# Kernel optimization log

Measured on AMD Instinct MI355X. Metric: run time of the kernel, lower is better.

## Reference

```python
import jax, jax.numpy as jnp
import numpy as np

EPS = 1e-5
KH = KW = 3
PAD = 1

def conv3x3(x, w, b=None):
    out = jax.lax.conv_general_dilated(
        x, w, window_strides=(1, 1), padding=((PAD, PAD), (PAD, PAD)),
        dimension_numbers=("NCHW", "OIHW", "NCHW"))
    if b is not None:
        out = out + b[None, :, None, None]
    return out

def batchnorm(x, gamma, beta):
    # training-mode BatchNorm2d: batch statistics over (N, H, W)
    mean = x.mean(axis=(0, 2, 3), keepdims=True)
    var = x.var(axis=(0, 2, 3), keepdims=True)
    return gamma[None, :, None, None] * (x - mean) / jnp.sqrt(var + EPS) + beta[None, :, None, None]

def bilinear_gather(x, y_pos, x_pos):
    # x: [B,C,H,W]; y_pos/x_pos: [B,P,H,W] (P = KH*KW sampling taps)
    # zero padding outside image (mmcv modulated deform conv semantics)
    B, C, H, W = x.shape
    P = y_pos.shape[1]
    x_flat = x.reshape(B, C, H * W)
    y0 = jnp.floor(y_pos)
    x0 = jnp.floor(x_pos)
    ly = y_pos - y0
    lx = x_pos - x0
    out = jnp.zeros((B, C, P, H, W), dtype=x.dtype)
    for dy, dx, wgt in ((0, 0, (1 - ly) * (1 - lx)), (0, 1, (1 - ly) * lx),
                        (1, 0, ly * (1 - lx)), (1, 1, ly * lx)):
        yi = y0 + dy
        xi = x0 + dx
        valid = ((yi >= 0) & (yi <= H - 1) & (xi >= 0) & (xi <= W - 1)).astype(x.dtype)
        yc = jnp.clip(yi, 0, H - 1).astype(jnp.int32)
        xc = jnp.clip(xi, 0, W - 1).astype(jnp.int32)
        idx = (yc * W + xc).reshape(B, 1, P * H * W)
        vals = jnp.take_along_axis(x_flat, jnp.broadcast_to(idx, (B, C, P * H * W)), axis=2)
        vals = vals.reshape(B, C, P, H, W)
        out = out + vals * (wgt * valid)[:, None]
    return out  # [B,C,P,H,W]

def modulated_deform_conv(x, w_off, b_off, w_dcn):
    B, C, H, W = x.shape
    P = KH * KW
    off = conv3x3(x, w_off, b_off)  # [B, 3*P, H, W]
    o1, o2, m = jnp.split(off, 3, axis=1)
    offset = jnp.concatenate([o1, o2], axis=1)            # [B, 2P, H, W]
    offset = offset.reshape(B, P, 2, H, W)                # channel 2p -> dy, 2p+1 -> dx
    mask = jax.nn.sigmoid(m)                              # [B, P, H, W]
    hh = jnp.arange(H, dtype=x.dtype)
    ww = jnp.arange(W, dtype=x.dtype)
    ky = jnp.arange(KH, dtype=x.dtype)
    kx = jnp.arange(KW, dtype=x.dtype)
    # base sampling grid per tap p = ky*KW + kx: (h - PAD + ky, w - PAD + kx)
    base_y = (hh[None, :] - PAD + ky[:, None])            # [KH, H]
    base_x = (ww[None, :] - PAD + kx[:, None])            # [KW, W]
    base_y = jnp.broadcast_to(base_y[:, None, :, None], (KH, KW, H, W)).reshape(P, H, W)
    base_x = jnp.broadcast_to(base_x[None, :, None, :], (KH, KW, H, W)).reshape(P, H, W)
    y_pos = base_y[None] + offset[:, :, 0]                # [B,P,H,W]
    x_pos = base_x[None] + offset[:, :, 1]
    sampled = bilinear_gather(x, y_pos, x_pos)            # [B,C,P,H,W]
    sampled = sampled * mask[:, None]
    w = w_dcn.reshape(w_dcn.shape[0], C, P)               # [O, C, P]
    return jnp.einsum("bcphw,ocp->bohw", sampled, w)

def setup_inputs() -> dict:
    key = jax.random.key(0)
    ks = jax.random.split(key, 10)
    B, Ch, H, W = 4, 256, 64, 64
    Cin, Cout = 2 * Ch, 256
    P = KH * KW
    inp = {
        "input_v": jax.random.normal(ks[0], (B, Ch, H, W), jnp.float32),
        "input_i": jax.random.normal(ks[1], (B, Ch, H, W), jnp.float32),
        "w_off": jax.random.normal(ks[2], (3 * P, Cin, KH, KW), jnp.float32) * 0.01,
        "b_off": jnp.zeros((3 * P,), jnp.float32),
        "w_dcn": jax.random.normal(ks[3], (Cout, Cin, KH, KW), jnp.float32) * (1.0 / np.sqrt(Cin * P)),
        "gamma1": jnp.ones((Cout,), jnp.float32),
        "beta1": jnp.zeros((Cout,), jnp.float32),
        "w2": jax.random.normal(ks[4], (Cout, Cout, KH, KW), jnp.float32) * (1.0 / np.sqrt(Cout * P)),
        "gamma2": jnp.ones((Cout,), jnp.float32),
        "beta2": jnp.zeros((Cout,), jnp.float32),
    }
    return inp

def reference(input_v, input_i, w_off, b_off, w_dcn, gamma1, beta1, w2, gamma2, beta2):
    x = jnp.concatenate([input_v, input_i], axis=1)
    out = modulated_deform_conv(x, w_off, b_off, w_dcn)
    out = jax.nn.relu(batchnorm(out, gamma1, beta1))
    out = jax.nn.relu(batchnorm(conv3x3(out, w2), gamma2, beta2))
    return out
```

## Files before the change

### kernel.cpp

```cpp
#include <hip/hip_runtime.h>
#include <cstdint>
#include <cstddef>

typedef unsigned short u16;
typedef __attribute__((ext_vector_type(8))) short s16x8;
typedef __attribute__((ext_vector_type(4))) float f32x4;

#define DEV __device__ __forceinline__

DEV float bf2f(short u){
  union { unsigned int i; float f; } v;
  v.i = ((unsigned int)(u16)u) << 16;
  return v.f;
}
DEV short f2bf(float f){
  union { float f; unsigned int i; } v; v.f = f;
  unsigned int u = v.i;
  u += 0x7fffu + ((u >> 16) & 1u);
  return (short)(u >> 16);
}
DEV s16x8 s16x8_zero(){
  s16x8 z;
#pragma unroll
  for(int j=0;j<8;j++) z[j]=0;
  return z;
}
DEV f32x4 f32x4_zero(){
  f32x4 z;
#pragma unroll
  for(int j=0;j<4;j++) z[j]=0.f;
  return z;
}
DEV f32x4 mfma16(s16x8 a, s16x8 b, f32x4 c){
  return __builtin_amdgcn_mfma_f32_16x16x32_bf16(a, b, c, 0, 0, 0);
}
DEV void bar_lds(){
  asm volatile("s_waitcnt lgkmcnt(0)");
  __builtin_amdgcn_s_barrier();
}
DEV void wait_vm4(){ asm volatile("s_waitcnt vmcnt(4)" ::: "memory"); }
DEV void wait_vm1(){ asm volatile("s_waitcnt vmcnt(1)" ::: "memory"); }
DEV void gload16(const u16* g, u16* l){
  __builtin_amdgcn_global_load_lds(
      (const __attribute__((address_space(1))) unsigned int*)g,
      (__attribute__((address_space(3))) unsigned int*)l, 16, 0, 0);
}

static constexpr size_t OFF_ACC_B  = 0;
static constexpr size_t STATS_B    = 2097152;
static constexpr size_t ZERO_BYTES = STATS_B + 4096;
static constexpr size_t OUT1_ACC_B = ZERO_BYTES;
static constexpr size_t OUT2_ACC_B = OUT1_ACC_B + 16777216;
static constexpr size_t XN_B       = OUT2_ACC_B + 16777216;
static constexpr size_t OUT1N_B    = XN_B + 16777216;
static constexpr size_t WOFFT_B    = OUT1N_B + 8388608;
static constexpr size_t WDCNT_B    = WOFFT_B + 294912;
static constexpr size_t W2T_B      = WDCNT_B + 2359296;

__global__ void k_x_to_nhwc(const float* __restrict__ v, const float* __restrict__ vi,
                            u16* __restrict__ xn){
  __shared__ float tile[64][65];
  const int b = blockIdx.z, c0 = blockIdx.y*64, hw0 = blockIdx.x*64;
  const float* src = (c0 < 256) ? (v  + ((size_t)b*256 + c0)      *4096)
                                : (vi + ((size_t)b*256 + (c0-256))*4096);
  const int t = threadIdx.x;
#pragma unroll
  for(int k=0;k<16;k++){
    int idx = t + k*256;
    int cl = idx >> 6, wl = idx & 63;
    tile[cl][wl] = src[(size_t)cl*4096 + hw0 + wl];
  }
  __syncthreads();
#pragma unroll
  for(int k=0;k<16;k++){
    int idx = t + k*256;
    int wl = idx >> 6, cl = idx & 63;
    xn[(size_t)(b*4096 + hw0 + wl)*512 + c0 + cl] = (u16)f2bf(tile[cl][wl]);
  }
}

__global__ void k_prep_woff(const float* __restrict__ w, u16* __restrict__ wt){
  int idx = blockIdx.x*256 + threadIdx.x;
  if(idx >= 32*4608) return;
  int n = idx / 4608, k = idx % 4608;
  int t = k >> 9, c = k & 511;
  float val = (n < 27) ? w[(size_t)(n*512 + c)*9 + t] : 0.f;
  wt[idx] = (u16)f2bf(val);
}
__global__ void k_prep_wdcn(const float* __restrict__ w, u16* __restrict__ wt){
  int idx = blockIdx.x*256 + threadIdx.x;
  if(idx >= 256*4608) return;
  int n = idx / 4608, k = idx % 4608;
  int t = k >> 9, c = k & 511;
  wt[idx] = (u16)f2bf(w[(size_t)(n*512 + c)*9 + t]);
}
__global__ void k_prep_w2(const float* __restrict__ w, u16* __restrict__ wt){
  int idx = blockIdx.x*256 + threadIdx.x;
  if(idx >= 256*2304) return;
  int n = idx / 2304, k = idx % 2304;
  int t = k >> 8, c = k & 255;
  wt[idx] = (u16)f2bf(w[(size_t)(n*256 + c)*9 + t]);
}

__global__ __launch_bounds__(256, 2) void k_conv_off(
    const u16* __restrict__ xn, const u16* __restrict__ wt, float* __restrict__ offa){
  __shared__ short A_lds[4][128][8];
  __shared__ short B_lds[4][32][8];
  const int tid = threadIdx.x;
  const int lane = tid & 63, wid = tid >> 6;
  const int quad = lane >> 4, ln = lane & 15;
  const int m0 = blockIdx.x * 128;
  const int b = m0 >> 12;
  const int h0 = (m0 & 4095) >> 6;
  const int ks = blockIdx.y;
  const int ts0 = (ks == 3) ? 6 : ks*2;
  const int ntap = (ks == 3) ? 3 : 2;
  const int m_base = wid * 32;
  const int r = tid >> 1, sp = (tid & 1) * 2;
  const int h_r = h0 + (r >> 6), w_r = r & 63;
  const s16x8* Ap = (const s16x8*)A_lds;
  const s16x8* Bp = (const s16x8*)B_lds;
  f32x4 acc[2][2];
#pragma unroll
  for(int mf=0;mf<2;mf++)
#pragma unroll
    for(int nf=0;nf<2;nf++) acc[mf][nf] = f32x4_zero();

  auto load_it = [&](int it, s16x8& v0, s16x8& v1, s16x8& bv){
    const int tp = ts0 + (it >> 4);
    const int cA = (it & 15)*32;
    const int ty = tp/3, tx = tp - ty*3;
    const int y = h_r - 1 + ty, x = w_r - 1 + tx;
    const bool vld = (y>=0) & (y<64) & (x>=0) & (x<64);
    v0 = s16x8_zero(); v1 = s16x8_zero();
    if(vld){
      const u16* src = xn + ((size_t)((b<<12) + (y<<6) + x) << 9) + cA + sp*8;
      v0 = *(const s16x8*)(src);
      v1 = *(const s16x8*)(src + 8);
    }
    if(tid < 128){
      const int n = tid & 31, s2 = tid >> 5;
      bv = *(const s16x8*)(wt + (size_t)n*4608 + tp*512 + cA + s2*8);
    }
  };

  const int NIT = ntap * 16;
  s16x8 v0a, v1a, bva, v0b, v1b, bvb;
  bva = s16x8_zero(); bvb = s16x8_zero();
  load_it(0, v0a, v1a, bva);
  load_it(1, v0b, v1b, bvb);
  for(int it = 0; it < NIT; it += 2){
    bar_lds();
    *(s16x8*)(&A_lds[sp][r][0])   = v0a;
    *(s16x8*)(&A_lds[sp+1][r][0]) = v1a;
    if(tid < 128){
      const int n = tid & 31, s2 = tid >> 5;
      *(s16x8*)(&B_lds[s2][n][0]) = bva;
    }
    if(it + 2 < NIT) load_it(it + 2, v0a, v1a, bva);
    bar_lds();
    {
      s16x8 a0 = Ap[quad*128 + m_base + ln];
      s16x8 a1 = Ap[quad*128 + m_base + 16 + ln];
      s16x8 b0 = Bp[quad*32 + ln];
      s16x8 b1 = Bp[quad*32 + 16 + ln];
      acc[0][0] = mfma16(a0, b0, acc[0][0]);
      acc[0][1] = mfma16(a0, b1, acc[0][1]);
      acc[1][0] = mfma16(a1, b0, acc[1][0]);
      acc[1][1] = mfma16(a1, b1, acc[1][1]);
    }
    bar_lds();
    *(s16x8*)(&A_lds[sp][r][0])   = v0b;
    *(s16x8*)(&A_lds[sp+1][r][0]) = v1b;
    if(tid < 128){
      const int n = tid & 31, s2 = tid >> 5;
      *(s16x8*)(&B_lds[s2][n][0]) = bvb;
    }
    if(it + 3 < NIT) load_it(it + 3, v0b, v1b, bvb);
    bar_lds();
    {
      s16x8 a0 = Ap[quad*128 + m_base + ln];
      s16x8 a1 = Ap[quad*128 + m_base + 16 + ln];
      s16x8 b0 = Bp[quad*32 + ln];
      s16x8 b1 = Bp[quad*32 + 16 + ln];
      acc[0][0] = mfma16(a0, b0, acc[0][0]);
      acc[0][1] = mfma16(a0, b1, acc[0][1]);
      acc[1][0] = mfma16(a1, b0, acc[1][0]);
      acc[1][1] = mfma16(a1, b1, acc[1][1]);
    }
  }
#pragma unroll
  for(int mf=0;mf<2;mf++)
#pragma unroll
    for(int nf=0;nf<2;nf++){
      const int col = nf*16 + ln;
#pragma unroll
      for(int i=0;i<4;i++){
        const int row = m_base + mf*16 + quad*4 + i;
        unsafeAtomicAdd(offa + (size_t)(m0+row)*32 + col, acc[mf][nf][i]);
      }
    }
}

__global__ __launch_bounds__(512, 1) void k_dcn(
    const u16* __restrict__ xn, const u16* __restrict__ wt,
    const float* __restrict__ offa, const float* __restrict__ boff,
    float* __restrict__ outa){
  __shared__ short A_lds[2][8][64][8];
  __shared__ short B_lds[2][8][256][8];
  __shared__ int   p_ofs[9][4][64];
  __shared__ float p_wgt[9][4][64];
  const int tid = threadIdx.x;
  const int lane = tid & 63, wid = tid >> 6;
  const int quad = lane >> 4, ln = lane & 15;
  const int wm = wid >> 2, wn = wid & 3;
  const int m0 = blockIdx.x * 64;
  const int b = m0 >> 12;
  const int h = (m0 & 4095) >> 6;
  const int r_s = tid >> 3, sub = tid & 7;
  constexpr int NP = 72;
  f32x4 acc[2][4];
#pragma unroll
  for(int mf=0;mf<2;mf++)
#pragma unroll
    for(int nf=0;nf<4;nf++) acc[mf][nf] = f32x4_zero();

  {
    const int rr = tid & 63;
    const float* orow = offa + (size_t)(m0+rr)*32;
    for(int tp = tid >> 6; tp < 9; tp += 8){
      float dy = orow[2*tp]   + boff[2*tp];
      float dx = orow[2*tp+1] + boff[2*tp+1];
      float mz = orow[18+tp]  + boff[18+tp];
      float mk = 1.f / (1.f + expf(-mz));
      float ypos = (float)(h - 1 + tp/3) + dy;
      float xpos = (float)(rr - 1 + tp%3) + dx;
      float y0f = floorf(ypos), x0f = floorf(xpos);
      float ly = ypos - y0f, lx = xpos - x0f;
      int y0 = (int)y0f, x0 = (int)x0f;
#pragma unroll
      for(int k=0;k<4;k++){
        int ddy = k >> 1, ddx = k & 1;
        int yi = y0 + ddy, xi = x0 + ddx;
        bool vv = (yi >= 0) & (yi < 64) & (xi >= 0) & (xi < 64);
        float wk = (ddy ? ly : 1.f-ly) * (ddx ? lx : 1.f-lx) * mk;
        if(!vv) wk = 0.f;
        int yc = yi < 0 ? 0 : (yi > 63 ? 63 : yi);
        int xc = xi < 0 ? 0 : (xi > 63 ? 63 : xi);
        p_ofs[tp][k][rr] = ((b << 12) + (yc << 6) + xc) << 9;
        p_wgt[tp][k][rr] = wk;
      }
    }
  }
  __syncthreads();

  auto gather = [&](int t, s16x8* g){
    const int tp = t >> 3;
    const int kcc = (t & 7)*64 + sub*8;
#pragma unroll
    for(int k=0;k<4;k++)
      g[k] = *(const s16x8*)(xn + p_ofs[tp][k][r_s] + kcc);
  };
  auto blendw = [&](int t, const s16x8* g){
    const int tp = t >> 3;
    const float w0 = p_wgt[tp][0][r_s], w1 = p_wgt[tp][1][r_s];
    const float w2 = p_wgt[tp][2][r_s], w3 = p_wgt[tp][3][r_s];
    s16x8 pk;
#pragma unroll
    for(int j=0;j<8;j++){
      float f = w0 * bf2f(g[0][j]);
      f = fmaf(w1, bf2f(g[1][j]), f);
      f = fmaf(w2, bf2f(g[2][j]), f);
      f = fmaf(w3, bf2f(g[3][j]), f);
      pk[j] = f2bf(f);
    }
    return pk;
  };
  auto stageB = [&](int t, int bi){
    const int tp = t >> 3, kc = (t & 7)*64;
#pragma unroll
    for(int i=0;i<4;i++){
      const int li = wid*4 + i;
      const int sl = li >> 2, n0 = (li & 3)*64;
      gload16(wt + (size_t)(n0 + lane)*4608 + tp*512 + kc + sl*8,
              (u16*)&B_lds[bi][sl][n0][0]);
    }
  };
  auto phase = [&](int t, int cur, const s16x8* gB, s16x8* gF){
    const int nxt = cur ^ 1;
    if(t + 1 < NP){
      s16x8 pk = blendw(t + 1, gB);
      *(s16x8*)&A_lds[nxt][sub][r_s][0] = pk;
      stageB(t + 1, nxt);
    }
    __builtin_amdgcn_sched_barrier(0);
    if(t + 2 < NP) gather(t + 2, gF);
#pragma unroll
    for(int kk=0;kk<2;kk++){
      s16x8 af0 = *(const s16x8*)&A_lds[cur][kk*4+quad][wm*32 + ln][0];
      s16x8 af1 = *(const s16x8*)&A_lds[cur][kk*4+quad][wm*32 + 16 + ln][0];
      s16x8 bf[4];
#pragma unroll
      for(int nf=0;nf<4;nf++)
        bf[nf] = *(const s16x8*)&B_lds[cur][kk*4+quad][wn*64 + nf*16 + ln][0];
#pragma unroll
      for(int nf=0;nf<4;nf++){
        acc[0][nf] = mfma16(af0, bf[nf], acc[0][nf]);
        acc[1][nf] = mfma16(af1, bf[nf], acc[1][nf]);
      }
    }
    wait_vm4();
    bar_lds();
  };

  s16x8 S0[4], S1[4];
  gather(0, S0);
  stageB(0, 0);
  __builtin_amdgcn_sched_barrier(0);
  gather(1, S1);
  {
    s16x8 pk = blendw(0, S0);
    *(s16x8*)&A_lds[0][sub][r_s][0] = pk;
  }
  wait_vm4();
  bar_lds();

  for(int t = 0; t < NP; t += 2){
    phase(t,     0, S1, S0);
    phase(t + 1, 1, S0, S1);
  }

#pragma unroll
  for(int mf=0;mf<2;mf++)
#pragma unroll
    for(int nf=0;nf<4;nf++){
      const int col = wn*64 + nf*16 + ln;
#pragma unroll
      for(int i=0;i<4;i++){
        const int row = m0 + wm*32 + mf*16 + quad*4 + i;
        outa[(size_t)row*256 + col] = acc[mf][nf][i];
      }
    }
}

__global__ __launch_bounds__(512, 1) void k_conv2(
    const u16* __restrict__ a_in, const u16* __restrict__ wt, float* __restrict__ outa){
  __shared__ short A_lds[2][8][64][8];
  __shared__ short B_lds[2][8][256][8];
  const int tid = threadIdx.x;
  const int lane = tid & 63, wid = tid >> 6;
  const int quad = lane >> 4, ln = lane & 15;
  const int wm = wid >> 2, wn = wid & 3;
  const int m0 = blockIdx.x * 64;
  const int b = m0 >> 12;
  const int h = (m0 & 4095) >> 6;
  const int r_s = tid >> 3, sub = tid & 7;
  constexpr int NP = 36;
  f32x4 acc[2][4];
#pragma unroll
  for(int mf=0;mf<2;mf++)
#pragma unroll
    for(int nf=0;nf<4;nf++) acc[mf][nf] = f32x4_zero();

  auto loadA = [&](int t, s16x8& va){
    const int tp = t >> 2;
    const int ty = tp/3, tx = tp - ty*3;
    const int y = h - 1 + ty, x = r_s - 1 + tx;
    const bool vld = (y>=0) & (y<64) & (x>=0) & (x<64);
    va = s16x8_zero();
    if(vld)
      va = *(const s16x8*)(a_in + (((size_t)((b<<12) + (y<<6) + x)) << 8)
                           + (t & 3)*64 + sub*8);
  };
  auto stageB = [&](int t, int bi){
    const int tp = t >> 2, kc = (t & 3)*64;
#pragma unroll
    for(int i=0;i<4;i++){
      const int li = wid*4 + i;
      const int sl = li >> 2, n0 = (li & 3)*64;
      gload16(wt + (size_t)(n0 + lane)*2304 + tp*256 + kc + sl*8,
              (u16*)&B_lds[bi][sl][n0][0]);
    }
  };
  auto phase = [&](int t, int cur, const s16x8& vB, s16x8& vF){
    const int nxt = cur ^ 1;
    if(t + 1 < NP){
      *(s16x8*)&A_lds[nxt][sub][r_s][0] = vB;
      stageB(t + 1, nxt);
    }
    __builtin_amdgcn_sched_barrier(0);
    if(t + 2 < NP) loadA(t + 2, vF);
#pragma unroll
    for(int kk=0;kk<2;kk++){
      s16x8 af0 = *(const s16x8*)&A_lds[cur][kk*4+quad][wm*32 + ln][0];
      s16x8 af1 = *(const s16x8*)&A_lds[cur][kk*4+quad][wm*32 + 16 + ln][0];
      s16x8 bf[4];
#pragma unroll
      for(int nf=0;nf<4;nf++)
        bf[nf] = *(const s16x8*)&B_lds[cur][kk*4+quad][wn*64 + nf*16 + ln][0];
#pragma unroll
      for(int nf=0;nf<4;nf++){
        acc[0][nf] = mfma16(af0, bf[nf], acc[0][nf]);
        acc[1][nf] = mfma16(af1, bf[nf], acc[1][nf]);
      }
    }
    wait_vm1();
    bar_lds();
  };

  s16x8 S0, S1;
  loadA(0, S0);
  stageB(0, 0);
  __builtin_amdgcn_sched_barrier(0);
  loadA(1, S1);
  *(s16x8*)&A_lds[0][sub][r_s][0] = S0;
  wait_vm1();
  bar_lds();

  for(int t = 0; t < NP; t += 2){
    phase(t,     0, S1, S0);
    phase(t + 1, 1, S0, S1);
  }

#pragma unroll
  for(int mf=0;mf<2;mf++)
#pragma unroll
    for(int nf=0;nf<4;nf++){
      const int col = wn*64 + nf*16 + ln;
#pragma unroll
      for(int i=0;i<4;i++){
        const int row = m0 + wm*32 + mf*16 + quad*4 + i;
        outa[(size_t)row*256 + col] = acc[mf][nf][i];
      }
    }
}

__global__ void k_stats(const float* __restrict__ acc, float* __restrict__ sum,
                        float* __restrict__ sq){
  const int m0 = blockIdx.x*64;
  const int c = threadIdx.x;
  float s = 0.f, q = 0.f;
  for(int i=0;i<64;i++){
    float v = acc[(size_t)(m0+i)*256 + c];
    s += v; q += v*v;
  }
  unsafeAtomicAdd(sum + c, s);
  unsafeAtomicAdd(sq + c, q);
}

__global__ void k_bn1(const float* __restrict__ acc, const float* __restrict__ sum,
                      const float* __restrict__ sq, const float* __restrict__ g,
                      const float* __restrict__ bt, u16* __restrict__ o){
  __shared__ float sc[256], sh[256];
  const int t = threadIdx.x;
  {
    float mean = sum[t] * (1.f/16384.f);
    float var  = sq[t] * (1.f/16384.f) - mean*mean;
    float rstd = rsqrtf(var + 1e-5f);
    float s = g[t] * rstd;
    sc[t] = s; sh[t] = bt[t] - mean*s;
  }
  __syncthreads();
  const int c4 = (t & 63) * 4;
  const float s0 = sc[c4], s1 = sc[c4+1], s2 = sc[c4+2], s3 = sc[c4+3];
  const float h0 = sh[c4], h1 = sh[c4+1], h2 = sh[c4+2], h3 = sh[c4+3];
#pragma unroll
  for(int k=0;k<4;k++){
    int m = blockIdx.x*16 + k*4 + (t>>6);
    const float4 v = *(const float4*)(acc + (size_t)m*256 + c4);
    unsigned int lo = (unsigned int)(u16)f2bf(fmaxf(0.f, v.x*s0 + h0))
                    | ((unsigned int)(u16)f2bf(fmaxf(0.f, v.y*s1 + h1)) << 16);
    unsigned int hi = (unsigned int)(u16)f2bf(fmaxf(0.f, v.z*s2 + h2))
                    | ((unsigned int)(u16)f2bf(fmaxf(0.f, v.w*s3 + h3)) << 16);
    uint2 pr; pr.x = lo; pr.y = hi;
    *(uint2*)(o + (size_t)m*256 + c4) = pr;
  }
}

__global__ void k_bn2_out(const float* __restrict__ acc, const float* __restrict__ sum,
                          const float* __restrict__ sq, const float* __restrict__ g,
                          const float* __restrict__ bt, float* __restrict__ out){
  __shared__ float tile[64][65];
  __shared__ float sc[64], sh[64];
  const int t = threadIdx.x;
  const int b = blockIdx.z, c0 = blockIdx.y*64, hw0 = blockIdx.x*64;
  if(t < 64){
    int c = c0 + t;
    float mean = sum[c] * (1.f/16384.f);
    float var  = sq[c] * (1.f/16384.f) - mean*mean;
    float rstd = rsqrtf(var + 1e-5f);
    float s = g[c] * rstd;
    sc[t] = s; sh[t] = bt[c] - mean*s;
  }
  __syncthreads();
#pragma unroll
  for(int k=0;k<16;k++){
    int idx = t + k*256;
    int wl = idx >> 6, cl = idx & 63;
    float v = acc[(size_t)((b<<12) + hw0 + wl)*256 + c0 + cl];
    tile[wl][cl] = fmaxf(0.f, v*sc[cl] + sh[cl]);
  }
  __syncthreads();
#pragma unroll
  for(int k=0;k<16;k++){
    int idx = t + k*256;
    int cl = idx >> 6, wl = idx & 63;
    out[(size_t)(b*256 + c0 + cl)*4096 + hw0 + wl] = tile[wl][cl];
  }
}

extern "C" void kernel_launch(void* const* d_in, const int* in_sizes, int n_in,
                              void* d_out, int out_size, void* d_ws, size_t ws_size,
                              hipStream_t stream){
  const float* in_v  = (const float*)d_in[0];
  const float* in_i  = (const float*)d_in[1];
  const float* w_off = (const float*)d_in[2];
  const float* b_off = (const float*)d_in[3];
  const float* w_dcn = (const float*)d_in[4];
  const float* g1    = (const float*)d_in[5];
  const float* bt1   = (const float*)d_in[6];
  const float* w2    = (const float*)d_in[7];
  const float* g2    = (const float*)d_in[8];
  const float* bt2   = (const float*)d_in[9];
  float* out = (float*)d_out;
  char* ws = (char*)d_ws;

  float* off_acc  = (float*)(ws + OFF_ACC_B);
  float* stats    = (float*)(ws + STATS_B);
  float* out1_acc = (float*)(ws + OUT1_ACC_B);
  float* out2_acc = (float*)(ws + OUT2_ACC_B);
  float* sum1 = stats,       *sq1 = stats + 256;
  float* sum2 = stats + 512, *sq2 = stats + 768;
  u16* xn    = (u16*)(ws + XN_B);
  u16* out1n = (u16*)(ws + OUT1N_B);
  u16* wofft = (u16*)(ws + WOFFT_B);
  u16* wdcnt = (u16*)(ws + WDCNT_B);
  u16* w2t   = (u16*)(ws + W2T_B);

  hipMemsetAsync(ws, 0, ZERO_BYTES, stream);
  k_x_to_nhwc<<<dim3(64,8,4), 256, 0, stream>>>(in_v, in_i, xn);
  k_prep_woff<<<576, 256, 0, stream>>>(w_off, wofft);
  k_prep_wdcn<<<4608, 256, 0, stream>>>(w_dcn, wdcnt);
  k_prep_w2<<<2304, 256, 0, stream>>>(w2, w2t);
  k_conv_off<<<dim3(128,4), 256, 0, stream>>>(xn, wofft, off_acc);
  k_dcn<<<256, 512, 0, stream>>>(xn, wdcnt, off_acc, b_off, out1_acc);
  k_stats<<<256, 256, 0, stream>>>(out1_acc, sum1, sq1);
  k_bn1<<<1024, 256, 0, stream>>>(out1_acc, sum1, sq1, g1, bt1, out1n);
  k_conv2<<<256, 512, 0, stream>>>(out1n, w2t, out2_acc);
  k_stats<<<256, 256, 0, stream>>>(out2_acc, sum2, sq2);
  k_bn2_out<<<dim3(64,4,4), 256, 0, stream>>>(out2_acc, sum2, sq2, g2, bt2, out);
}
```

Before: 367.9 us.

## Split deformable conv into sampling pass plus split-K GEMMs over padded NHWC inputs

Replaces the fused gather+GEMM deformable conv kernel with three steps: a per-pixel offset/weight precompute kernel, a sampling kernel that writes a bf16 im2col matrix S to global memory, and a plain GEMM. Both GEMMs are retiled to 256-thread blocks with N and K splits, reduced through float atomics. The inputs to the convolutions are stored with a one-pixel zero border so bounds checks disappear. The goal is more parallelism and simpler GEMM loops. The cost is a large extra write and read of the im2col matrix, more atomic traffic, and a single-buffered GEMM loop that no longer overlaps loads with compute.

```diff
diff --git a/kernel.cpp b/kernel.cpp
--- a/kernel.cpp
+++ b/kernel.cpp
@@ -38,29 +38,31 @@
   asm volatile("s_waitcnt lgkmcnt(0)");
   __builtin_amdgcn_s_barrier();
 }
-DEV void wait_vm4(){ asm volatile("s_waitcnt vmcnt(4)" ::: "memory"); }
-DEV void wait_vm1(){ asm volatile("s_waitcnt vmcnt(1)" ::: "memory"); }
 DEV void gload16(const u16* g, u16* l){
   __builtin_amdgcn_global_load_lds(
       (const __attribute__((address_space(1))) unsigned int*)g,
       (__attribute__((address_space(3))) unsigned int*)l, 16, 0, 0);
 }
 
-static constexpr size_t OFF_ACC_B  = 0;
-static constexpr size_t STATS_B    = 2097152;
-static constexpr size_t ZERO_BYTES = STATS_B + 4096;
-static constexpr size_t OUT1_ACC_B = ZERO_BYTES;
-static constexpr size_t OUT2_ACC_B = OUT1_ACC_B + 16777216;
-static constexpr size_t XN_B       = OUT2_ACC_B + 16777216;
-static constexpr size_t OUT1N_B    = XN_B + 16777216;
-static constexpr size_t WOFFT_B    = OUT1N_B + 8388608;
-static constexpr size_t WDCNT_B    = WOFFT_B + 294912;
-static constexpr size_t W2T_B      = WDCNT_B + 2359296;
+static constexpr size_t OFF_ACC_B   = 0;
+static constexpr size_t STATS_B     = 2097152;
+static constexpr size_t OUT1_ACC_B  = 2101248;
+static constexpr size_t OUT2_ACC_B  = 18878464;
+static constexpr size_t XN_PAD_B    = 35655680;
+static constexpr size_t OUT1N_PAD_B = 53497856;
+static constexpr size_t ZERO_BYTES  = 62418944;
+static constexpr size_t S_B         = 62418944;
+static constexpr size_t WOFFT_B     = 213708800;
+static constexpr size_t WDCNT_B     = 214003712;
+static constexpr size_t W2T_B       = 216363008;
+static constexpr size_t POFS_B      = 217542656;
+static constexpr size_t PWGT_B      = 219901952;
 
 __global__ void k_x_to_nhwc(const float* __restrict__ v, const float* __restrict__ vi,
                             u16* __restrict__ xn){
   __shared__ float tile[64][65];
   const int b = blockIdx.z, c0 = blockIdx.y*64, hw0 = blockIdx.x*64;
+  const int h = hw0 >> 6;
   const float* src = (c0 < 256) ? (v  + ((size_t)b*256 + c0)      *4096)
                                 : (vi + ((size_t)b*256 + (c0-256))*4096);
   const int t = threadIdx.x;
@@ -75,7 +77,7 @@
   for(int k=0;k<16;k++){
     int idx = t + k*256;
     int wl = idx >> 6, cl = idx & 63;
-    xn[(size_t)(b*4096 + hw0 + wl)*512 + c0 + cl] = (u16)f2bf(tile[cl][wl]);
+    xn[((size_t)(b*66 + h+1)*66 + wl+1)*512 + c0 + cl] = (u16)f2bf(tile[cl][wl]);
   }
 }
 
@@ -130,14 +132,10 @@
     const int tp = ts0 + (it >> 4);
     const int cA = (it & 15)*32;
     const int ty = tp/3, tx = tp - ty*3;
-    const int y = h_r - 1 + ty, x = w_r - 1 + tx;
-    const bool vld = (y>=0) & (y<64) & (x>=0) & (x<64);
-    v0 = s16x8_zero(); v1 = s16x8_zero();
-    if(vld){
-      const u16* src = xn + ((size_t)((b<<12) + (y<<6) + x) << 9) + cA + sp*8;
-      v0 = *(const s16x8*)(src);
-      v1 = *(const s16x8*)(src + 8);
-    }
+    const int y = h_r + ty, x = w_r + tx;
+    const u16* src = xn + ((size_t)(b*66 + y)*66 + x)*512 + cA + sp*8;
+    v0 = *(const s16x8*)(src);
+    v1 = *(const s16x8*)(src + 8);
     if(tid < 128){
       const int n = tid & 31, s2 = tid >> 5;
       bv = *(const s16x8*)(wt + (size_t)n*4608 + tp*512 + cA + s2*8);
@@ -202,235 +200,184 @@
     }
 }
 
-__global__ __launch_bounds__(512, 1) void k_dcn(
-    const u16* __restrict__ xn, const u16* __restrict__ wt,
-    const float* __restrict__ offa, const float* __restrict__ boff,
-    float* __restrict__ outa){
-  __shared__ short A_lds[2][8][64][8];
-  __shared__ short B_lds[2][8][256][8];
-  __shared__ int   p_ofs[9][4][64];
-  __shared__ float p_wgt[9][4][64];
+__global__ void k_prep_off2(const float* __restrict__ offa, const float* __restrict__ boff,
+                            int* __restrict__ pofs, float* __restrict__ pwgt){
+  int id = blockIdx.x*256 + threadIdx.x;
+  if(id >= 16384*9) return;
+  int m = id / 9, tp = id - m*9;
+  int b = m >> 12, h = (m >> 6) & 63, w = m & 63;
+  const float* orow = offa + (size_t)m*32;
+  float dy = orow[2*tp]   + boff[2*tp];
+  float dx = orow[2*tp+1] + boff[2*tp+1];
+  float mz = orow[18+tp]  + boff[18+tp];
+  float mk = 1.f / (1.f + expf(-mz));
+  float ypos = (float)(h - 1 + tp/3) + dy;
+  float xpos = (float)(w - 1 + tp%3) + dx;
+  float y0f = floorf(ypos), x0f = floorf(xpos);
+  float ly = ypos - y0f, lx = xpos - x0f;
+  int y0 = (int)y0f, x0 = (int)x0f;
+#pragma unroll
+  for(int k=0;k<4;k++){
+    int ddy = k >> 1, ddx = k & 1;
+    int yi = y0 + ddy, xi = x0 + ddx;
+    int yc = yi < -1 ? -1 : (yi > 64 ? 64 : yi);
+    int xc = xi < -1 ? -1 : (xi > 64 ? 64 : xi);
+    float wk = (ddy ? ly : 1.f-ly) * (ddx ? lx : 1.f-lx) * mk;
+    pofs[id*4+k] = ((b*66 + yc+1)*66 + xc+1) << 9;
+    pwgt[id*4+k] = wk;
+  }
+}
+
+__global__ __launch_bounds__(256) void k_sample(
+    const u16* __restrict__ xn, const int* __restrict__ pofs,
+    const float* __restrict__ pwgt, u16* __restrict__ S){
+  const int wid = threadIdx.x >> 6, lane = threadIdx.x & 63;
+  const int m = blockIdx.x*4 + wid;
+  const int tp = blockIdx.y;
+  const int id4 = (m*9 + tp)*4;
+  const int4   of = *(const int4*)  (pofs + id4);
+  const float4 wg = *(const float4*)(pwgt + id4);
+  const int c0 = lane*8;
+  s16x8 g0 = *(const s16x8*)(xn + of.x + c0);
+  s16x8 g1 = *(const s16x8*)(xn + of.y + c0);
+  s16x8 g2 = *(const s16x8*)(xn + of.z + c0);
+  s16x8 g3 = *(const s16x8*)(xn + of.w + c0);
+  s16x8 pk;
+#pragma unroll
+  for(int j=0;j<8;j++){
+    float f = wg.x * bf2f(g0[j]);
+    f = fmaf(wg.y, bf2f(g1[j]), f);
+    f = fmaf(wg.z, bf2f(g2[j]), f);
+    f = fmaf(wg.w, bf2f(g3[j]), f);
+    pk[j] = f2bf(f);
+  }
+  *(s16x8*)(S + (size_t)m*4608 + tp*512 + c0) = pk;
+}
+
+__global__ __launch_bounds__(256, 4) void k_gemm1(
+    const u16* __restrict__ S, const u16* __restrict__ wt, float* __restrict__ outa){
+  __shared__ short A_lds[8][64][8];
+  __shared__ short B_lds[8][128][8];
   const int tid = threadIdx.x;
   const int lane = tid & 63, wid = tid >> 6;
   const int quad = lane >> 4, ln = lane & 15;
-  const int wm = wid >> 2, wn = wid & 3;
+  const int wm = wid >> 1, wn = wid & 1;
   const int m0 = blockIdx.x * 64;
-  const int b = m0 >> 12;
-  const int h = (m0 & 4095) >> 6;
-  const int r_s = tid >> 3, sub = tid & 7;
-  constexpr int NP = 72;
+  const int n0 = blockIdx.y * 128;
+  const int kbase = blockIdx.z * 2304;
+  const u16* Arow = S + (size_t)(m0 + lane)*4608;
   f32x4 acc[2][4];
 #pragma unroll
   for(int mf=0;mf<2;mf++)
 #pragma unroll
     for(int nf=0;nf<4;nf++) acc[mf][nf] = f32x4_zero();
 
-  {
-    const int rr = tid & 63;
-    const float* orow = offa + (size_t)(m0+rr)*32;
-    for(int tp = tid >> 6; tp < 9; tp += 8){
-      float dy = orow[2*tp]   + boff[2*tp];
-      float dx = orow[2*tp+1] + boff[2*tp+1];
-      float mz = orow[18+tp]  + boff[18+tp];
-      float mk = 1.f / (1.f + expf(-mz));
-      float ypos = (float)(h - 1 + tp/3) + dy;
-      float xpos = (float)(rr - 1 + tp%3) + dx;
-      float y0f = floorf(ypos), x0f = floorf(xpos);
-      float ly = ypos - y0f, lx = xpos - x0f;
-      int y0 = (int)y0f, x0 = (int)x0f;
-#pragma unroll
-      for(int k=0;k<4;k++){
-        int ddy = k >> 1, ddx = k & 1;
-        int yi = y0 + ddy, xi = x0 + ddx;
-        bool vv = (yi >= 0) & (yi < 64) & (xi >= 0) & (xi < 64);
-        float wk = (ddy ? ly : 1.f-ly) * (ddx ? lx : 1.f-lx) * mk;
-        if(!vv) wk = 0.f;
-        int yc = yi < 0 ? 0 : (yi > 63 ? 63 : yi);
-        int xc = xi < 0 ? 0 : (xi > 63 ? 63 : xi);
-        p_ofs[tp][k][rr] = ((b << 12) + (yc << 6) + xc) << 9;
-        p_wgt[tp][k][rr] = wk;
-      }
-    }
-  }
-  __syncthreads();
-
-  auto gather = [&](int t, s16x8* g){
-    const int tp = t >> 3;
-    const int kcc = (t & 7)*64 + sub*8;
-#pragma unroll
-    for(int k=0;k<4;k++)
-      g[k] = *(const s16x8*)(xn + p_ofs[tp][k][r_s] + kcc);
-  };
-  auto blendw = [&](int t, const s16x8* g){
-    const int tp = t >> 3;
-    const float w0 = p_wgt[tp][0][r_s], w1 = p_wgt[tp][1][r_s];
-    const float w2 = p_wgt[tp][2][r_s], w3 = p_wgt[tp][3][r_s];
-    s16x8 pk;
-#pragma unroll
-    for(int j=0;j<8;j++){
-      float f = w0 * bf2f(g[0][j]);
-      f = fmaf(w1, bf2f(g[1][j]), f);
-      f = fmaf(w2, bf2f(g[2][j]), f);
-      f = fmaf(w3, bf2f(g[3][j]), f);
-      pk[j] = f2bf(f);
-    }
-    return pk;
-  };
-  auto stageB = [&](int t, int bi){
-    const int tp = t >> 3, kc = (t & 7)*64;
+  for(int t = 0; t < 36; ++t){
+    const int k0 = kbase + t*64;
+#pragma unroll
+    for(int i=0;i<2;i++){
+      const int g = wid*2 + i;
+      gload16(Arow + k0 + g*8, (u16*)&A_lds[g][0][0]);
+    }
 #pragma unroll
     for(int i=0;i<4;i++){
-      const int li = wid*4 + i;
-      const int sl = li >> 2, n0 = (li & 3)*64;
-      gload16(wt + (size_t)(n0 + lane)*4608 + tp*512 + kc + sl*8,
-              (u16*)&B_lds[bi][sl][n0][0]);
-    }
-  };
-  auto phase = [&](int t, int cur, const s16x8* gB, s16x8* gF){
-    const int nxt = cur ^ 1;
-    if(t + 1 < NP){
-      s16x8 pk = blendw(t + 1, gB);
-      *(s16x8*)&A_lds[nxt][sub][r_s][0] = pk;
-      stageB(t + 1, nxt);
-    }
-    __builtin_amdgcn_sched_barrier(0);
-    if(t + 2 < NP) gather(t + 2, gF);
+      const int g2 = wid*4 + i;
+      gload16(wt + (size_t)(n0 + (g2&1)*64 + lane)*4608 + k0 + (g2>>1)*8,
+              (u16*)&B_lds[g2>>1][(g2&1)*64][0]);
+    }
+    __syncthreads();
 #pragma unroll
     for(int kk=0;kk<2;kk++){
-      s16x8 af0 = *(const s16x8*)&A_lds[cur][kk*4+quad][wm*32 + ln][0];
-      s16x8 af1 = *(const s16x8*)&A_lds[cur][kk*4+quad][wm*32 + 16 + ln][0];
-      s16x8 bf[4];
+      s16x8 af[2], bf[4];
+#pragma unroll
+      for(int mf=0;mf<2;mf++)
+        af[mf] = *(const s16x8*)&A_lds[kk*4+quad][wm*32 + mf*16 + ln][0];
 #pragma unroll
       for(int nf=0;nf<4;nf++)
-        bf[nf] = *(const s16x8*)&B_lds[cur][kk*4+quad][wn*64 + nf*16 + ln][0];
-#pragma unroll
-      for(int nf=0;nf<4;nf++){
-        acc[0][nf] = mfma16(af0, bf[nf], acc[0][nf]);
-        acc[1][nf] = mfma16(af1, bf[nf], acc[1][nf]);
-      }
-    }
-    wait_vm4();
-    bar_lds();
-  };
-
-  s16x8 S0[4], S1[4];
-  gather(0, S0);
-  stageB(0, 0);
-  __builtin_amdgcn_sched_barrier(0);
-  gather(1, S1);
-  {
-    s16x8 pk = blendw(0, S0);
-    *(s16x8*)&A_lds[0][sub][r_s][0] = pk;
-  }
-  wait_vm4();
-  bar_lds();
-
-  for(int t = 0; t < NP; t += 2){
-    phase(t,     0, S1, S0);
-    phase(t + 1, 1, S0, S1);
-  }
-
+        bf[nf] = *(const s16x8*)&B_lds[kk*4+quad][wn*64 + nf*16 + ln][0];
+#pragma unroll
+      for(int mf=0;mf<2;mf++)
+#pragma unroll
+        for(int nf=0;nf<4;nf++)
+          acc[mf][nf] = mfma16(af[mf], bf[nf], acc[mf][nf]);
+    }
+    __syncthreads();
+  }
 #pragma unroll
   for(int mf=0;mf<2;mf++)
 #pragma unroll
     for(int nf=0;nf<4;nf++){
-      const int col = wn*64 + nf*16 + ln;
+      const int col = n0 + wn*64 + nf*16 + ln;
 #pragma unroll
       for(int i=0;i<4;i++){
         const int row = m0 + wm*32 + mf*16 + quad*4 + i;
-        outa[(size_t)row*256 + col] = acc[mf][nf][i];
+        unsafeAtomicAdd(outa + (size_t)row*256 + col, acc[mf][nf][i]);
       }
     }
 }
 
-__global__ __launch_bounds__(512, 1) void k_conv2(
-    const u16* __restrict__ a_in, const u16* __restrict__ wt, float* __restrict__ outa){
-  __shared__ short A_lds[2][8][64][8];
-  __shared__ short B_lds[2][8][256][8];
+__global__ __launch_bounds__(256, 4) void k_gemm2(
+    const u16* __restrict__ a_pad, const u16* __restrict__ wt, float* __restrict__ outa){
+  __shared__ short A_lds[8][64][8];
+  __shared__ short B_lds[8][128][8];
   const int tid = threadIdx.x;
   const int lane = tid & 63, wid = tid >> 6;
   const int quad = lane >> 4, ln = lane & 15;
-  const int wm = wid >> 2, wn = wid & 3;
+  const int wm = wid >> 1, wn = wid & 1;
   const int m0 = blockIdx.x * 64;
+  const int n0 = blockIdx.y * 128;
+  const int kbase = blockIdx.z * 1152;
   const int b = m0 >> 12;
   const int h = (m0 & 4095) >> 6;
-  const int r_s = tid >> 3, sub = tid & 7;
-  constexpr int NP = 36;
   f32x4 acc[2][4];
 #pragma unroll
   for(int mf=0;mf<2;mf++)
 #pragma unroll
     for(int nf=0;nf<4;nf++) acc[mf][nf] = f32x4_zero();
 
-  auto loadA = [&](int t, s16x8& va){
-    const int tp = t >> 2;
+  for(int t = 0; t < 18; ++t){
+    const int k0 = kbase + t*64;
+    const int tp = k0 >> 8, cit = k0 & 255;
     const int ty = tp/3, tx = tp - ty*3;
-    const int y = h - 1 + ty, x = r_s - 1 + tx;
-    const bool vld = (y>=0) & (y<64) & (x>=0) & (x<64);
-    va = s16x8_zero();
-    if(vld)
-      va = *(const s16x8*)(a_in + (((size_t)((b<<12) + (y<<6) + x)) << 8)
-                           + (t & 3)*64 + sub*8);
-  };
-  auto stageB = [&](int t, int bi){
-    const int tp = t >> 2, kc = (t & 3)*64;
+    const u16* Arow = a_pad + ((size_t)(b*66 + h + ty)*66 + lane + tx)*256 + cit;
+#pragma unroll
+    for(int i=0;i<2;i++){
+      const int g = wid*2 + i;
+      gload16(Arow + g*8, (u16*)&A_lds[g][0][0]);
+    }
 #pragma unroll
     for(int i=0;i<4;i++){
-      const int li = wid*4 + i;
-      const int sl = li >> 2, n0 = (li & 3)*64;
-      gload16(wt + (size_t)(n0 + lane)*2304 + tp*256 + kc + sl*8,
-              (u16*)&B_lds[bi][sl][n0][0]);
-    }
-  };
-  auto phase = [&](int t, int cur, const s16x8& vB, s16x8& vF){
-    const int nxt = cur ^ 1;
-    if(t + 1 < NP){
-      *(s16x8*)&A_lds[nxt][sub][r_s][0] = vB;
-      stageB(t + 1, nxt);
-    }
-    __builtin_amdgcn_sched_barrier(0);
-    if(t + 2 < NP) loadA(t + 2, vF);
+      const int g2 = wid*4 + i;
+      gload16(wt + (size_t)(n0 + (g2&1)*64 + lane)*2304 + k0 + (g2>>1)*8,
+              (u16*)&B_lds[g2>>1][(g2&1)*64][0]);
+    }
+    __syncthreads();
 #pragma unroll
     for(int kk=0;kk<2;kk++){
-      s16x8 af0 = *(const s16x8*)&A_lds[cur][kk*4+quad][wm*32 + ln][0];
-      s16x8 af1 = *(const s16x8*)&A_lds[cur][kk*4+quad][wm*32 + 16 + ln][0];
-      s16x8 bf[4];
+      s16x8 af[2], bf[4];
+#pragma unroll
+      for(int mf=0;mf<2;mf++)
+        af[mf] = *(const s16x8*)&A_lds[kk*4+quad][wm*32 + mf*16 + ln][0];
 #pragma unroll
       for(int nf=0;nf<4;nf++)
-        bf[nf] = *(const s16x8*)&B_lds[cur][kk*4+quad][wn*64 + nf*16 + ln][0];
-#pragma unroll
-      for(int nf=0;nf<4;nf++){
-        acc[0][nf] = mfma16(af0, bf[nf], acc[0][nf]);
-        acc[1][nf] = mfma16(af1, bf[nf], acc[1][nf]);
-      }
-    }
-    wait_vm1();
-    bar_lds();
-  };
-
-  s16x8 S0, S1;
-  loadA(0, S0);
-  stageB(0, 0);
-  __builtin_amdgcn_sched_barrier(0);
-  loadA(1, S1);
-  *(s16x8*)&A_lds[0][sub][r_s][0] = S0;
-  wait_vm1();
-  bar_lds();
-
-  for(int t = 0; t < NP; t += 2){
-    phase(t,     0, S1, S0);
-    phase(t + 1, 1, S0, S1);
-  }
-
+        bf[nf] = *(const s16x8*)&B_lds[kk*4+quad][wn*64 + nf*16 + ln][0];
+#pragma unroll
+      for(int mf=0;mf<2;mf++)
+#pragma unroll
+        for(int nf=0;nf<4;nf++)
+          acc[mf][nf] = mfma16(af[mf], bf[nf], acc[mf][nf]);
+    }
+    __syncthreads();
+  }
 #pragma unroll
   for(int mf=0;mf<2;mf++)
 #pragma unroll
     for(int nf=0;nf<4;nf++){
-      const int col = wn*64 + nf*16 + ln;
+      const int col = n0 + wn*64 + nf*16 + ln;
 #pragma unroll
       for(int i=0;i<4;i++){
         const int row = m0 + wm*32 + mf*16 + quad*4 + i;
-        outa[(size_t)row*256 + col] = acc[mf][nf][i];
+        unsafeAtomicAdd(outa + (size_t)row*256 + col, acc[mf][nf][i]);
       }
     }
 }
@@ -467,13 +414,14 @@
 #pragma unroll
   for(int k=0;k<4;k++){
     int m = blockIdx.x*16 + k*4 + (t>>6);
+    int b = m >> 12, hh = (m >> 6) & 63, ww = m & 63;
     const float4 v = *(const float4*)(acc + (size_t)m*256 + c4);
     unsigned int lo = (unsigned int)(u16)f2bf(fmaxf(0.f, v.x*s0 + h0))
                     | ((unsigned int)(u16)f2bf(fmaxf(0.f, v.y*s1 + h1)) << 16);
     unsigned int hi = (unsigned int)(u16)f2bf(fmaxf(0.f, v.z*s2 + h2))
                     | ((unsigned int)(u16)f2bf(fmaxf(0.f, v.w*s3 + h3)) << 16);
     uint2 pr; pr.x = lo; pr.y = hi;
-    *(uint2*)(o + (size_t)m*256 + c4) = pr;
+    *(uint2*)(o + ((size_t)(b*66 + hh+1)*66 + ww+1)*256 + c4) = pr;
   }
 }
 
@@ -525,28 +473,33 @@
   float* out = (float*)d_out;
   char* ws = (char*)d_ws;
 
-  float* off_acc  = (float*)(ws + OFF_ACC_B);
-  float* stats    = (float*)(ws + STATS_B);
-  float* out1_acc = (float*)(ws + OUT1_ACC_B);
-  float* out2_acc = (float*)(ws + OUT2_ACC_B);
+  float* off_acc   = (float*)(ws + OFF_ACC_B);
+  float* stats     = (float*)(ws + STATS_B);
+  float* out1_acc  = (float*)(ws + OUT1_ACC_B);
+  float* out2_acc  = (float*)(ws + OUT2_ACC_B);
+  u16*   xn_pad    = (u16*)  (ws + XN_PAD_B);
+  u16*   out1n_pad = (u16*)  (ws + OUT1N_PAD_B);
+  u16*   Smat      = (u16*)  (ws + S_B);
+  u16*   wofft     = (u16*)  (ws + WOFFT_B);
+  u16*   wdcnt     = (u16*)  (ws + WDCNT_B);
+  u16*   w2t       = (u16*)  (ws + W2T_B);
+  int*   pofs      = (int*)  (ws + POFS_B);
+  float* pwgt      = (float*)(ws + PWGT_B);
   float* sum1 = stats,       *sq1 = stats + 256;
   float* sum2 = stats + 512, *sq2 = stats + 768;
-  u16* xn    = (u16*)(ws + XN_B);
-  u16* out1n = (u16*)(ws + OUT1N_B);
-  u16* wofft = (u16*)(ws + WOFFT_B);
-  u16* wdcnt = (u16*)(ws + WDCNT_B);
-  u16* w2t   = (u16*)(ws + W2T_B);
 
   hipMemsetAsync(ws, 0, ZERO_BYTES, stream);
-  k_x_to_nhwc<<<dim3(64,8,4), 256, 0, stream>>>(in_v, in_i, xn);
+  k_x_to_nhwc<<<dim3(64,8,4), 256, 0, stream>>>(in_v, in_i, xn_pad);
   k_prep_woff<<<576, 256, 0, stream>>>(w_off, wofft);
   k_prep_wdcn<<<4608, 256, 0, stream>>>(w_dcn, wdcnt);
   k_prep_w2<<<2304, 256, 0, stream>>>(w2, w2t);
-  k_conv_off<<<dim3(128,4), 256, 0, stream>>>(xn, wofft, off_acc);
-  k_dcn<<<256, 512, 0, stream>>>(xn, wdcnt, off_acc, b_off, out1_acc);
+  k_conv_off<<<dim3(128,4), 256, 0, stream>>>(xn_pad, wofft, off_acc);
+  k_prep_off2<<<576, 256, 0, stream>>>(off_acc, b_off, pofs, pwgt);
+  k_sample<<<dim3(4096,9), 256, 0, stream>>>(xn_pad, pofs, pwgt, Smat);
+  k_gemm1<<<dim3(256,2,2), 256, 0, stream>>>(Smat, wdcnt, out1_acc);
   k_stats<<<256, 256, 0, stream>>>(out1_acc, sum1, sq1);
-  k_bn1<<<1024, 256, 0, stream>>>(out1_acc, sum1, sq1, g1, bt1, out1n);
-  k_conv2<<<256, 512, 0, stream>>>(out1n, w2t, out2_acc);
+  k_bn1<<<1024, 256, 0, stream>>>(out1_acc, sum1, sq1, g1, bt1, out1n_pad);
+  k_gemm2<<<dim3(256,2,2), 256, 0, stream>>>(out1n_pad, w2t, out2_acc);
   k_stats<<<256, 256, 0, stream>>>(out2_acc, sum2, sq2);
   k_bn2_out<<<dim3(64,4,4), 256, 0, stream>>>(out2_acc, sum2, sq2, g2, bt2, out);
 }
```

New measurement: 428.3 us. 1.16x slower.
